# Kernel optimization log

Measured on AMD Instinct MI355X. Metric: run time of the kernel, lower is better.

## Reference

```python
import jax, jax.numpy as jnp
import numpy as np

B, L, H_IN = 2, 512, 768
E = 256          # hidden_size
N = 12           # num_labels


def setup_inputs() -> dict:
    key = jax.random.key(0)
    ks = jax.random.split(key, 10)
    lim_in = 1.0 / np.sqrt(H_IN)
    lim_e = 1.0 / np.sqrt(E)
    lim_2e = 1.0 / np.sqrt(2 * E)
    return {
        "x":    jax.random.normal(ks[0], (B, L, H_IN), dtype=jnp.float32),
        "sW":   jax.random.uniform(ks[1], (E, H_IN), jnp.float32, -lim_in, lim_in),
        "sb":   jax.random.uniform(ks[2], (E,), jnp.float32, -lim_in, lim_in),
        "tW":   jax.random.uniform(ks[3], (E, H_IN), jnp.float32, -lim_in, lim_in),
        "tb":   jax.random.uniform(ks[4], (E,), jnp.float32, -lim_in, lim_in),
        "f2W":  jax.random.uniform(ks[5], (E, 2 * E), jnp.float32, -lim_2e, lim_2e),
        "f2b":  jax.random.uniform(ks[6], (E,), jnp.float32, -lim_2e, lim_2e),
        "f3W":  jax.random.normal(ks[7], (N, E), dtype=jnp.float32),  # init_weights: normal_
        "f3b":  jax.random.uniform(ks[8], (N,), jnp.float32, -lim_e, lim_e),
        "blW":  jax.random.normal(ks[9], (E * N, E), dtype=jnp.float32),  # bi_linear, no bias
    }


def reference(x, sW, sb, tW, tb, f2W, f2b, f3W, f3b, blW):
    b, l, _ = x.shape
    s = jax.nn.relu(x @ sW.T + sb)  # [B,L,E]
    t = jax.nn.relu(x @ tW.T + tb)  # [B,L,E]
    # biaffine term: key[b,s,e,n] = (s @ blW.T) reshaped, then key @ t^T
    key = (s @ blW.T).reshape(b, l, E, N)             # [B,L,E,N]
    out1 = jnp.einsum('bsen,ble->bsnl', key, t)       # [B,S,N,L]
    # pairwise concat-MLP, decomposed: cat(u,v) @ f2W.T == u@Wu.T + v@Wv.T
    Wu, Wv = f2W[:, :E], f2W[:, E:]
    su = s @ Wu.T                                     # [B,L,E]
    tv = t @ Wv.T                                     # [B,L,E]
    h = jax.nn.relu(su[:, :, None, :] + tv[:, None, :, :] + f2b)  # [B,L,L,E]
    out2 = h @ f3W.T + f3b                            # [B,L,L,N]
    out2 = jnp.transpose(out2, (0, 1, 3, 2))          # [B,L,N,L]
    return out1 + out2
```

## Files before the change

kernel.cpp:

```cpp
#include <hip/hip_runtime.h>
#include <hip/hip_bf16.h>


typedef unsigned short u16;
typedef __attribute__((ext_vector_type(8))) short    s16x8;
typedef __attribute__((ext_vector_type(8))) _Float16 f16x8;
typedef __attribute__((ext_vector_type(4))) float    f32x4;

__device__ inline u16 f2h(float f) { return __builtin_bit_cast(u16, (_Float16)f); }

__device__ inline s16x8 cvt2(float4 a, float4 b) {
    f16x8 h;
    h[0] = (_Float16)a.x; h[1] = (_Float16)a.y; h[2] = (_Float16)a.z; h[3] = (_Float16)a.w;
    h[4] = (_Float16)b.x; h[5] = (_Float16)b.y; h[6] = (_Float16)b.z; h[7] = (_Float16)b.w;
    return __builtin_bit_cast(s16x8, h);
}

__device__ inline f32x4 mfma_f16(s16x8 a, s16x8 b, f32x4 c) {
    return __builtin_amdgcn_mfma_f32_16x16x32_f16(
        __builtin_bit_cast(f16x8, a), __builtin_bit_cast(f16x8, b), c, 0, 0, 0);
}
__device__ inline f32x4 mfma_f16v(f16x8 a, s16x8 b, f32x4 c) {
    return __builtin_amdgcn_mfma_f32_16x16x32_f16(a, __builtin_bit_cast(f16x8, b), c, 0, 0, 0);
}

__global__ __launch_bounds__(256)
void conv_kernel(const float* __restrict__ f2W, const float* __restrict__ blW,
                 const float* __restrict__ f3W,
                 u16* __restrict__ blkw, u16* __restrict__ f3wb)
{
    int idx = blockIdx.x * 256 + threadIdx.x;
    if (idx >= 230400) return;
    float4 v;
    u16* dst;
    if (idx < 229376) {
        int i4 = idx * 4;
        int r = i4 >> 8, k = i4 & 255;
        const float* src;
        if (r < 3072)      { int n = r >> 8, e = r & 255; src = &blW[(e * 12 + n) * 256 + k]; }
        else if (r < 3328) { src = &f2W[(r - 3072) * 512 + k]; }
        else               { src = &f2W[(r - 3328) * 512 + 256 + k]; }
        v = *(const float4*)src;
        dst = &blkw[i4];
    } else {
        int i4 = (idx - 229376) * 4;
        int row = i4 >> 8, e = i4 & 255;
        if (row < 12) v = *(const float4*)&f3W[row * 256 + e];
        else          v = make_float4(0.f, 0.f, 0.f, 0.f);
        dst = &f3wb[i4];
    }
    ushort4 o;
    o.x = f2h(v.x); o.y = f2h(v.y); o.z = f2h(v.z); o.w = f2h(v.w);
    *(ushort4*)dst = o;
}

__global__ __launch_bounds__(256, 2)
void gemm_st(const float* __restrict__ x, const float* __restrict__ sW,
             const float* __restrict__ tW, const float* __restrict__ sb,
             const float* __restrict__ tb, u16* __restrict__ STb)
{
    __shared__ u16 As[64 * 72];
    __shared__ u16 Bs[64 * 72];
    const int tid = threadIdx.x;
    const int m0 = blockIdx.y * 64, n0 = blockIdx.x * 64;
    const int w = tid >> 6, l = tid & 63;
    const int wr = (w >> 1) * 32, wc = (w & 1) * 32;
    const int lr = l & 15, lg = l >> 4;
    const int srow = tid >> 2, kq = tid & 3;

    const float* ap = &x[(size_t)(m0 + srow) * 768 + kq * 16];
    int brow = n0 + srow;
    const float* bp = (brow < 256) ? &sW[(size_t)brow * 768 + kq * 16]
                                   : &tW[(size_t)(brow - 256) * 768 + kq * 16];
    float4 ra0 = *(const float4*)(ap + 0),  ra1 = *(const float4*)(ap + 4);
    float4 ra2 = *(const float4*)(ap + 8),  ra3 = *(const float4*)(ap + 12);
    float4 rb0 = *(const float4*)(bp + 0),  rb1 = *(const float4*)(bp + 4);
    float4 rb2 = *(const float4*)(bp + 8),  rb3 = *(const float4*)(bp + 12);

    f32x4 acc[2][2] = {};
    for (int k0 = 0; k0 < 768; k0 += 64) {
        __syncthreads();
        *(s16x8*)&As[srow * 72 + kq * 16]     = cvt2(ra0, ra1);
        *(s16x8*)&As[srow * 72 + kq * 16 + 8] = cvt2(ra2, ra3);
        *(s16x8*)&Bs[srow * 72 + kq * 16]     = cvt2(rb0, rb1);
        *(s16x8*)&Bs[srow * 72 + kq * 16 + 8] = cvt2(rb2, rb3);
        __syncthreads();
        if (k0 + 64 < 768) {
            ra0 = *(const float4*)(ap + k0 + 64 + 0);  ra1 = *(const float4*)(ap + k0 + 64 + 4);
            ra2 = *(const float4*)(ap + k0 + 64 + 8);  ra3 = *(const float4*)(ap + k0 + 64 + 12);
            rb0 = *(const float4*)(bp + k0 + 64 + 0);  rb1 = *(const float4*)(bp + k0 + 64 + 4);
            rb2 = *(const float4*)(bp + k0 + 64 + 8);  rb3 = *(const float4*)(bp + k0 + 64 + 12);
        }
#pragma unroll
        for (int kk = 0; kk < 64; kk += 32) {
            s16x8 af[2], bf[2];
            af[0] = *(const s16x8*)&As[(wr      + lr) * 72 + kk + lg * 8];
            af[1] = *(const s16x8*)&As[(wr + 16 + lr) * 72 + kk + lg * 8];
            bf[0] = *(const s16x8*)&Bs[(wc      + lr) * 72 + kk + lg * 8];
            bf[1] = *(const s16x8*)&Bs[(wc + 16 + lr) * 72 + kk + lg * 8];
#pragma unroll
            for (int fi = 0; fi < 2; ++fi)
#pragma unroll
                for (int fj = 0; fj < 2; ++fj)
                    acc[fi][fj] = mfma_f16(af[fi], bf[fj], acc[fi][fj]);
        }
    }
#pragma unroll
    for (int fi = 0; fi < 2; ++fi) {
#pragma unroll
        for (int fj = 0; fj < 2; ++fj) {
#pragma unroll
            for (int r = 0; r < 4; ++r) {
                int grow = m0 + wr + fi * 16 + lg * 4 + r;
                int gcol = n0 + wc + fj * 16 + lr;
                float bias = (gcol < 256) ? sb[gcol] : tb[gcol - 256];
                float v = fmaxf(acc[fi][fj][r] + bias, 0.f);
                STb[(size_t)grow * 512 + gcol] = f2h(v);
            }
        }
    }
}

__global__ __launch_bounds__(256, 2)
void gemm_kst(const u16* __restrict__ STb, const u16* __restrict__ BLKW,
              const float* __restrict__ f2b,
              u16* __restrict__ KEYP, u16* __restrict__ SUp, u16* __restrict__ TVp)
{
    __shared__ u16 As[64 * 72];
    __shared__ u16 Bs[64 * 72];
    const int tid = threadIdx.x;
    const int m0 = blockIdx.y * 64, n0 = blockIdx.x * 64;
    const int w = tid >> 6, l = tid & 63;
    const int wr = (w >> 1) * 32, wc = (w & 1) * 32;
    const int lr = l & 15, lg = l >> 4;
    const int srow = tid >> 2, kq = tid & 3;

    const u16* A = STb + (n0 >= 3328 ? 256 : 0);
    const u16* ap = &A[(size_t)(m0 + srow) * 512];
    const u16* bp = &BLKW[(size_t)(n0 + srow) * 256];
    s16x8 ra0 = *(const s16x8*)&ap[kq * 8];
    s16x8 ra1 = *(const s16x8*)&ap[(kq + 4) * 8];
    s16x8 rb0 = *(const s16x8*)&bp[kq * 8];
    s16x8 rb1 = *(const s16x8*)&bp[(kq + 4) * 8];

    f32x4 acc[2][2] = {};
    for (int k0 = 0; k0 < 256; k0 += 64) {
        __syncthreads();
        *(s16x8*)&As[srow * 72 + kq * 8]       = ra0;
        *(s16x8*)&As[srow * 72 + (kq + 4) * 8] = ra1;
        *(s16x8*)&Bs[srow * 72 + kq * 8]       = rb0;
        *(s16x8*)&Bs[srow * 72 + (kq + 4) * 8] = rb1;
        __syncthreads();
        if (k0 + 64 < 256) {
            ra0 = *(const s16x8*)&ap[k0 + 64 + kq * 8];
            ra1 = *(const s16x8*)&ap[k0 + 64 + (kq + 4) * 8];
            rb0 = *(const s16x8*)&bp[k0 + 64 + kq * 8];
            rb1 = *(const s16x8*)&bp[k0 + 64 + (kq + 4) * 8];
        }
#pragma unroll
        for (int kk = 0; kk < 64; kk += 32) {
            s16x8 af[2], bf[2];
            af[0] = *(const s16x8*)&As[(wr      + lr) * 72 + kk + lg * 8];
            af[1] = *(const s16x8*)&As[(wr + 16 + lr) * 72 + kk + lg * 8];
            bf[0] = *(const s16x8*)&Bs[(wc      + lr) * 72 + kk + lg * 8];
            bf[1] = *(const s16x8*)&Bs[(wc + 16 + lr) * 72 + kk + lg * 8];
#pragma unroll
            for (int fi = 0; fi < 2; ++fi)
#pragma unroll
                for (int fj = 0; fj < 2; ++fj)
                    acc[fi][fj] = mfma_f16(af[fi], bf[fj], acc[fi][fj]);
        }
    }
#pragma unroll
    for (int fi = 0; fi < 2; ++fi) {
#pragma unroll
        for (int fj = 0; fj < 2; ++fj) {
#pragma unroll
            for (int r = 0; r < 4; ++r) {
                int grow = m0 + wr + fi * 16 + lg * 4 + r;
                int gcol = n0 + wc + fj * 16 + lr;
                float v = acc[fi][fj][r];
                if (gcol < 3072) {
                    int n = gcol >> 8, e = gcol & 255;
                    KEYP[(size_t)n * 262144 + (size_t)grow * 256 + e] = f2h(v);
                } else if (gcol < 3328) {
                    SUp[(size_t)grow * 256 + (gcol - 3072)] = f2h(v);
                } else {
                    TVp[(size_t)grow * 256 + (gcol - 3328)] = f2h(v + f2b[gcol - 3328]);
                }
            }
        }
    }
}

__global__ __launch_bounds__(256, 4)
void fused_out(const u16* __restrict__ KEYP, const u16* __restrict__ STb,
               const u16* __restrict__ SUp, const u16* __restrict__ TVp,
               const u16* __restrict__ F3WH, const float* __restrict__ f3b,
               float* __restrict__ out)
{
    __shared__ __align__(16) char smem[30208];
    u16* lds = (u16*)smem;
    const int KEYC = 0, TC = 7680, SUC = 8960, TVC = 9600, F3C = 10880;

    const int tid = threadIdx.x;
    const int w = tid >> 6, l = tid & 63;

    const int lin  = blockIdx.x + (blockIdx.y << 4) + (blockIdx.z << 9);
    const int orig = (lin & 7) * 128 + (lin >> 3);
    const int j0 = (orig & 15) * 32;
    const int i0 = ((orig >> 4) & 31) * 16;
    const int b  = orig >> 9;

    const int lr = l & 15, lg = l >> 4;

    const u16* sb_[5]; int do_[5];
#pragma unroll
    for (int rr = 0; rr < 5; ++rr) {
        int g = tid + 256 * rr;
        const u16* s = nullptr; int d = 0;
        if (g < 768) {
            int n = g >> 6, ii = (g >> 2) & 15, qq = g & 3;
            s = KEYP + (size_t)n * 262144 + (size_t)(b * 512 + i0 + ii) * 256 + qq * 8;
            d = KEYC + (n * 16 + ii) * 40 + qq * 8;
        } else if (g < 896) {
            int q = g - 768, jj = q >> 2, qq = q & 3;
            s = STb + (size_t)(b * 512 + j0 + jj) * 512 + 256 + qq * 8;
            d = TC + jj * 40 + qq * 8;
        } else if (g < 960) {
            int q = g - 896, ii = q >> 2, qq = q & 3;
            s = SUp + (size_t)(b * 512 + i0 + ii) * 256 + qq * 8;
            d = SUC + ii * 40 + qq * 8;
        } else {
            int q = g - 960, jj = q >> 2, qq = q & 3;
            s = TVp + (size_t)(b * 512 + j0 + jj) * 256 + qq * 8;
            d = TVC + jj * 40 + qq * 8;
        }
        sb_[rr] = s; do_[rr] = d;
    }
    const bool v4 = (tid < 64);

#pragma unroll
    for (int rr = 0; rr < 2; ++rr) {
        int g = tid + 256 * rr;
        int row = g >> 5, qq = g & 31;
        *(s16x8*)&lds[F3C + row * 264 + qq * 8] = *(const s16x8*)&F3WH[row * 256 + qq * 8];
    }

    s16x8 st0, st1, st2, st3, st4 = {};
    f32x4 acc1[3][2] = {};
    f32x4 acc2[8]    = {};

    st0 = *(const s16x8*)(sb_[0]);
    st1 = *(const s16x8*)(sb_[1]);
    st2 = *(const s16x8*)(sb_[2]);
    st3 = *(const s16x8*)(sb_[3]);
    if (v4) st4 = *(const s16x8*)(sb_[4]);

    for (int it = 0; it < 8; ++it) {
        const int e0 = it * 32;
        __syncthreads();
        *(s16x8*)&lds[do_[0]] = st0;
        *(s16x8*)&lds[do_[1]] = st1;
        *(s16x8*)&lds[do_[2]] = st2;
        *(s16x8*)&lds[do_[3]] = st3;
        if (v4) *(s16x8*)&lds[do_[4]] = st4;
        __syncthreads();
        if (it < 7) {
            st0 = *(const s16x8*)(sb_[0] + e0 + 32);
            st1 = *(const s16x8*)(sb_[1] + e0 + 32);
            st2 = *(const s16x8*)(sb_[2] + e0 + 32);
            st3 = *(const s16x8*)(sb_[3] + e0 + 32);
            if (v4) st4 = *(const s16x8*)(sb_[4] + e0 + 32);
        }
        s16x8 tf0 = *(const s16x8*)&lds[TC + lr * 40 + lg * 8];
        s16x8 tf1 = *(const s16x8*)&lds[TC + (16 + lr) * 40 + lg * 8];
#pragma unroll
        for (int a = 0; a < 3; ++a) {
            int n = 3 * w + a;
            s16x8 kf = *(const s16x8*)&lds[KEYC + (n * 16 + lr) * 40 + lg * 8];
            acc1[a][0] = mfma_f16(kf, tf0, acc1[a][0]);
            acc1[a][1] = mfma_f16(kf, tf1, acc1[a][1]);
        }
        f16x8 sv = __builtin_bit_cast(f16x8, *(const s16x8*)&lds[SUC + lr * 40 + lg * 8]);
        s16x8 f3fr = *(const s16x8*)&lds[F3C + lr * 264 + e0 + lg * 8];
#pragma unroll
        for (int jj = 0; jj < 8; ++jj) {
            int j = w * 8 + jj;
            f16x8 tv8 = __builtin_bit_cast(f16x8, *(const s16x8*)&lds[TVC + j * 40 + lg * 8]);
            f16x8 hv = sv + tv8;
#pragma unroll
            for (int q = 0; q < 8; ++q)
                hv[q] = hv[q] > (_Float16)0.f ? hv[q] : (_Float16)0.f;
            acc2[jj] = mfma_f16v(hv, f3fr, acc2[jj]);
        }
    }

    __syncthreads();
    float* mg = (float*)smem;
    if (lr < 12) {
#pragma unroll
        for (int r = 0; r < 4; ++r) {
            int i = lg * 4 + r;
            f32x4 v0, v1;
            v0[0] = acc2[0][r]; v0[1] = acc2[1][r]; v0[2] = acc2[2][r]; v0[3] = acc2[3][r];
            v1[0] = acc2[4][r]; v1[1] = acc2[5][r]; v1[2] = acc2[6][r]; v1[3] = acc2[7][r];
            *(f32x4*)&mg[lr * 580 + i * 36 + w * 8]     = v0;
            *(f32x4*)&mg[lr * 580 + i * 36 + w * 8 + 4] = v1;
        }
    }
    __syncthreads();
#pragma unroll
    for (int a = 0; a < 3; ++a) {
        int n = 3 * w + a;
        float fb = f3b[n];
#pragma unroll
        for (int fj = 0; fj < 2; ++fj) {
            int j = fj * 16 + lr;
#pragma unroll
            for (int r = 0; r < 4; ++r) {
                int i = lg * 4 + r;
                float vv = acc1[a][fj][r] + mg[n * 580 + i * 36 + j] + fb;
                out[(((size_t)(b * 512 + i0 + i)) * 12 + n) * 512 + j0 + j] = vv;
            }
        }
    }
}

extern "C" void kernel_launch(void* const* d_in, const int* in_sizes, int n_in,
                              void* d_out, int out_size, void* d_ws, size_t ws_size,
                              hipStream_t stream)
{
    const float* x   = (const float*)d_in[0];
    const float* sW  = (const float*)d_in[1];
    const float* sb  = (const float*)d_in[2];
    const float* tW  = (const float*)d_in[3];
    const float* tb  = (const float*)d_in[4];
    const float* f2W = (const float*)d_in[5];
    const float* f2b = (const float*)d_in[6];
    const float* f3W = (const float*)d_in[7];
    const float* f3b = (const float*)d_in[8];
    const float* blW = (const float*)d_in[9];
    float* out = (float*)d_out;

    char* p = (char*)d_ws;
    u16* STb   = (u16*)p; p += 1048576;
    u16* blkw  = (u16*)p; p += 1835008;
    u16* KEYP  = (u16*)p; p += 6291456;
    u16* SUp   = (u16*)p; p += 524288;
    u16* TVp   = (u16*)p; p += 524288;
    u16* f3wbg = (u16*)p; p += 8192;

    conv_kernel<<<900, 256, 0, stream>>>(f2W, blW, f3W, blkw, f3wbg);
    gemm_st <<<dim3(8, 16),  256, 0, stream>>>(x, sW, tW, sb, tb, STb);
    gemm_kst<<<dim3(56, 16), 256, 0, stream>>>(STb, blkw, f2b, KEYP, SUp, TVp);
    fused_out<<<dim3(16, 32, 2), 256, 0, stream>>>(KEYP, STb, SUp, TVp, f3wbg, f3b, out);
}
```

Baseline: 52.08 us.

## Merge weight conversion and S/T projection GEMM into one launch with smaller tiles

The weight fp32-to-fp16 conversion kernel and the x·[sW;tW] GEMM are combined into a single launch. The first 256 blocks run the GEMM, which now uses 64x32 tiles to give more blocks, and the remaining blocks do the conversion. This removes one kernel launch and lets the two independent jobs overlap. The gemm_kst launch bound is also raised to 4 blocks per CU for occupancy, which may force register spills. Half of the threads now sit idle while B is staged.

```diff
diff --git a/kernel.cpp b/kernel.cpp
--- a/kernel.cpp
+++ b/kernel.cpp
@@ -24,104 +24,105 @@
     return __builtin_amdgcn_mfma_f32_16x16x32_f16(a, __builtin_bit_cast(f16x8, b), c, 0, 0, 0);
 }
 
-__global__ __launch_bounds__(256)
-void conv_kernel(const float* __restrict__ f2W, const float* __restrict__ blW,
-                 const float* __restrict__ f3W,
-                 u16* __restrict__ blkw, u16* __restrict__ f3wb)
+__global__ __launch_bounds__(256, 2)
+void prep_kernel(const float* __restrict__ x, const float* __restrict__ sW,
+                 const float* __restrict__ tW, const float* __restrict__ sb,
+                 const float* __restrict__ tb, const float* __restrict__ f2W,
+                 const float* __restrict__ blW, const float* __restrict__ f3W,
+                 u16* __restrict__ STb, u16* __restrict__ blkw, u16* __restrict__ f3wb)
 {
-    int idx = blockIdx.x * 256 + threadIdx.x;
-    if (idx >= 230400) return;
-    float4 v;
-    u16* dst;
-    if (idx < 229376) {
-        int i4 = idx * 4;
-        int r = i4 >> 8, k = i4 & 255;
-        const float* src;
-        if (r < 3072)      { int n = r >> 8, e = r & 255; src = &blW[(e * 12 + n) * 256 + k]; }
-        else if (r < 3328) { src = &f2W[(r - 3072) * 512 + k]; }
-        else               { src = &f2W[(r - 3328) * 512 + 256 + k]; }
-        v = *(const float4*)src;
-        dst = &blkw[i4];
-    } else {
-        int i4 = (idx - 229376) * 4;
-        int row = i4 >> 8, e = i4 & 255;
-        if (row < 12) v = *(const float4*)&f3W[row * 256 + e];
-        else          v = make_float4(0.f, 0.f, 0.f, 0.f);
-        dst = &f3wb[i4];
-    }
-    ushort4 o;
-    o.x = f2h(v.x); o.y = f2h(v.y); o.z = f2h(v.z); o.w = f2h(v.w);
-    *(ushort4*)dst = o;
-}
-
-__global__ __launch_bounds__(256, 2)
-void gemm_st(const float* __restrict__ x, const float* __restrict__ sW,
-             const float* __restrict__ tW, const float* __restrict__ sb,
-             const float* __restrict__ tb, u16* __restrict__ STb)
-{
+    if (blockIdx.x >= 256) {
+        int idx = (blockIdx.x - 256) * 256 + threadIdx.x;
+        float4 v;
+        u16* dst;
+        if (idx < 229376) {
+            int i4 = idx * 4;
+            int r = i4 >> 8, k = i4 & 255;
+            const float* src;
+            if (r < 3072)      { int n = r >> 8, e = r & 255; src = &blW[(e * 12 + n) * 256 + k]; }
+            else if (r < 3328) { src = &f2W[(r - 3072) * 512 + k]; }
+            else               { src = &f2W[(r - 3328) * 512 + 256 + k]; }
+            v = *(const float4*)src;
+            dst = &blkw[i4];
+        } else {
+            int i4 = (idx - 229376) * 4;
+            int row = i4 >> 8, e = i4 & 255;
+            if (row < 12) v = *(const float4*)&f3W[row * 256 + e];
+            else          v = make_float4(0.f, 0.f, 0.f, 0.f);
+            dst = &f3wb[i4];
+        }
+        ushort4 o;
+        o.x = f2h(v.x); o.y = f2h(v.y); o.z = f2h(v.z); o.w = f2h(v.w);
+        *(ushort4*)dst = o;
+        return;
+    }
     __shared__ u16 As[64 * 72];
-    __shared__ u16 Bs[64 * 72];
+    __shared__ u16 Bs[32 * 72];
     const int tid = threadIdx.x;
-    const int m0 = blockIdx.y * 64, n0 = blockIdx.x * 64;
+    const int m0 = (blockIdx.x >> 4) * 64, n0 = (blockIdx.x & 15) * 32;
     const int w = tid >> 6, l = tid & 63;
-    const int wr = (w >> 1) * 32, wc = (w & 1) * 32;
+    const int wr = (w >> 1) * 32, wc = (w & 1) * 16;
     const int lr = l & 15, lg = l >> 4;
     const int srow = tid >> 2, kq = tid & 3;
 
     const float* ap = &x[(size_t)(m0 + srow) * 768 + kq * 16];
-    int brow = n0 + srow;
-    const float* bp = (brow < 256) ? &sW[(size_t)brow * 768 + kq * 16]
-                                   : &tW[(size_t)(brow - 256) * 768 + kq * 16];
+    const bool bstg = (tid < 128);
+    const float* bp = nullptr;
+    if (bstg) {
+        int br = n0 + (tid >> 2);
+        bp = (br < 256) ? &sW[(size_t)br * 768 + kq * 16]
+                        : &tW[(size_t)(br - 256) * 768 + kq * 16];
+    }
     float4 ra0 = *(const float4*)(ap + 0),  ra1 = *(const float4*)(ap + 4);
     float4 ra2 = *(const float4*)(ap + 8),  ra3 = *(const float4*)(ap + 12);
-    float4 rb0 = *(const float4*)(bp + 0),  rb1 = *(const float4*)(bp + 4);
-    float4 rb2 = *(const float4*)(bp + 8),  rb3 = *(const float4*)(bp + 12);
-
-    f32x4 acc[2][2] = {};
+    float4 rb0, rb1, rb2, rb3;
+    if (bstg) {
+        rb0 = *(const float4*)(bp + 0);  rb1 = *(const float4*)(bp + 4);
+        rb2 = *(const float4*)(bp + 8);  rb3 = *(const float4*)(bp + 12);
+    }
+
+    f32x4 acc[2] = {};
     for (int k0 = 0; k0 < 768; k0 += 64) {
         __syncthreads();
         *(s16x8*)&As[srow * 72 + kq * 16]     = cvt2(ra0, ra1);
         *(s16x8*)&As[srow * 72 + kq * 16 + 8] = cvt2(ra2, ra3);
-        *(s16x8*)&Bs[srow * 72 + kq * 16]     = cvt2(rb0, rb1);
-        *(s16x8*)&Bs[srow * 72 + kq * 16 + 8] = cvt2(rb2, rb3);
+        if (bstg) {
+            *(s16x8*)&Bs[(tid >> 2) * 72 + kq * 16]     = cvt2(rb0, rb1);
+            *(s16x8*)&Bs[(tid >> 2) * 72 + kq * 16 + 8] = cvt2(rb2, rb3);
+        }
         __syncthreads();
         if (k0 + 64 < 768) {
             ra0 = *(const float4*)(ap + k0 + 64 + 0);  ra1 = *(const float4*)(ap + k0 + 64 + 4);
             ra2 = *(const float4*)(ap + k0 + 64 + 8);  ra3 = *(const float4*)(ap + k0 + 64 + 12);
-            rb0 = *(const float4*)(bp + k0 + 64 + 0);  rb1 = *(const float4*)(bp + k0 + 64 + 4);
-            rb2 = *(const float4*)(bp + k0 + 64 + 8);  rb3 = *(const float4*)(bp + k0 + 64 + 12);
+            if (bstg) {
+                rb0 = *(const float4*)(bp + k0 + 64 + 0);  rb1 = *(const float4*)(bp + k0 + 64 + 4);
+                rb2 = *(const float4*)(bp + k0 + 64 + 8);  rb3 = *(const float4*)(bp + k0 + 64 + 12);
+            }
         }
 #pragma unroll
         for (int kk = 0; kk < 64; kk += 32) {
-            s16x8 af[2], bf[2];
+            s16x8 af[2], bf;
             af[0] = *(const s16x8*)&As[(wr      + lr) * 72 + kk + lg * 8];
             af[1] = *(const s16x8*)&As[(wr + 16 + lr) * 72 + kk + lg * 8];
-            bf[0] = *(const s16x8*)&Bs[(wc      + lr) * 72 + kk + lg * 8];
-            bf[1] = *(const s16x8*)&Bs[(wc + 16 + lr) * 72 + kk + lg * 8];
-#pragma unroll
-            for (int fi = 0; fi < 2; ++fi)
-#pragma unroll
-                for (int fj = 0; fj < 2; ++fj)
-                    acc[fi][fj] = mfma_f16(af[fi], bf[fj], acc[fi][fj]);
+            bf    = *(const s16x8*)&Bs[(wc      + lr) * 72 + kk + lg * 8];
+            acc[0] = mfma_f16(af[0], bf, acc[0]);
+            acc[1] = mfma_f16(af[1], bf, acc[1]);
         }
     }
 #pragma unroll
     for (int fi = 0; fi < 2; ++fi) {
 #pragma unroll
-        for (int fj = 0; fj < 2; ++fj) {
-#pragma unroll
-            for (int r = 0; r < 4; ++r) {
-                int grow = m0 + wr + fi * 16 + lg * 4 + r;
-                int gcol = n0 + wc + fj * 16 + lr;
-                float bias = (gcol < 256) ? sb[gcol] : tb[gcol - 256];
-                float v = fmaxf(acc[fi][fj][r] + bias, 0.f);
-                STb[(size_t)grow * 512 + gcol] = f2h(v);
-            }
-        }
-    }
-}
-
-__global__ __launch_bounds__(256, 2)
+        for (int r = 0; r < 4; ++r) {
+            int grow = m0 + wr + fi * 16 + lg * 4 + r;
+            int gcol = n0 + wc + lr;
+            float bias = (gcol < 256) ? sb[gcol] : tb[gcol - 256];
+            float v = fmaxf(acc[fi][r] + bias, 0.f);
+            STb[(size_t)grow * 512 + gcol] = f2h(v);
+        }
+    }
+}
+
+__global__ __launch_bounds__(256, 4)
 void gemm_kst(const u16* __restrict__ STb, const u16* __restrict__ BLKW,
               const float* __restrict__ f2b,
               u16* __restrict__ KEYP, u16* __restrict__ SUp, u16* __restrict__ TVp)
@@ -351,8 +352,8 @@
     u16* TVp   = (u16*)p; p += 524288;
     u16* f3wbg = (u16*)p; p += 8192;
 
-    conv_kernel<<<900, 256, 0, stream>>>(f2W, blW, f3W, blkw, f3wbg);
-    gemm_st <<<dim3(8, 16),  256, 0, stream>>>(x, sW, tW, sb, tb, STb);
+    prep_kernel<<<1156, 256, 0, stream>>>(x, sW, tW, sb, tb, f2W, blW, f3W,
+                                          STb, blkw, f3wbg);
     gemm_kst<<<dim3(56, 16), 256, 0, stream>>>(STb, blkw, f2b, KEYP, SUp, TVp);
     fused_out<<<dim3(16, 32, 2), 256, 0, stream>>>(KEYP, STb, SUp, TVp, f3wbg, f3b, out);
 }
```

New measurement: 46.43 us. 10.8% less time.
